# Kernel tuning notes

Hardware: AMD Instinct MI355X
Metric: run time of the kernel (lower is better)

## Reference

```python
import jax, jax.numpy as jnp
import numpy as np

N = 100000       # num nodes
E = 1600000      # num edges (avg degree 16)
IN_DIM = 256
EMB_DIM = 128
K = 2            # nlayers: number of propagation steps


def setup_inputs() -> dict:
    key = jax.random.key(0)
    k1, k2, k3, k4, k5 = jax.random.split(key, 5)
    x = jax.random.normal(k1, (N, IN_DIM), dtype=jnp.float32)
    # glorot-initialized linear weight + zero bias
    scale = jnp.sqrt(6.0 / (IN_DIM + EMB_DIM))
    W = jax.random.uniform(k2, (IN_DIM, EMB_DIM), minval=-scale, maxval=scale, dtype=jnp.float32)
    b = jnp.zeros((EMB_DIM,), dtype=jnp.float32)
    edge_src = jax.random.randint(k3, (E,), 0, N, dtype=jnp.int32)
    edge_dst = jax.random.randint(k4, (E,), 0, N, dtype=jnp.int32)
    # normalized-adjacency-like edge weights (positive, ~1/deg scale)
    edge_w = jax.random.uniform(k5, (E,), dtype=jnp.float32) * (1.0 / 16.0)
    return {"x": x, "W": W, "b": b, "edge_src": edge_src, "edge_dst": edge_dst, "edge_w": edge_w}


def reference(x, W, b, edge_src, edge_dst, edge_w):
    # dropout is identity in eval mode; linear + relu
    h = jax.nn.relu(x @ W + b)  # [N, EMB_DIM]
    # k-step sparse propagation: h <- g @ h, g given as COO edge list
    for _ in range(K):
        msg = h[edge_src] * edge_w[:, None]                     # [E, EMB_DIM]
        h = jax.ops.segment_sum(msg, edge_dst, num_segments=N)  # [N, EMB_DIM]
    return h
```

## Files before the change

### kernel.cpp

```cpp
#include <hip/hip_runtime.h>

#define IN_DIM 256
#define EMB 128
#define BKT_SHIFT 9
#define BKT_NODES 512
#define BINE 4096
#define SCAP 12288

typedef __attribute__((ext_vector_type(8))) short short8;
typedef __attribute__((ext_vector_type(4))) float f32x4;

__device__ __forceinline__ unsigned short bf16rtne(float f) {
    unsigned int u = __float_as_uint(f);
    return (unsigned short)((u + 0x7fffu + ((u >> 16) & 1u)) >> 16);
}

__device__ __forceinline__ unsigned int packbf2(float lo, float hi) {
    return ((unsigned int)bf16rtne(hi) << 16) | (unsigned int)bf16rtne(lo);
}

__device__ __forceinline__ short8 pack8(float4 f0, float4 f1) {
    union { uint4 u; short8 s; } U;
    asm("v_cvt_pk_bf16_f32 %0, %1, %2" : "=v"(U.u.x) : "v"(f0.x), "v"(f0.y));
    asm("v_cvt_pk_bf16_f32 %0, %1, %2" : "=v"(U.u.y) : "v"(f0.z), "v"(f0.w));
    asm("v_cvt_pk_bf16_f32 %0, %1, %2" : "=v"(U.u.z) : "v"(f1.x), "v"(f1.y));
    asm("v_cvt_pk_bf16_f32 %0, %1, %2" : "=v"(U.u.w) : "v"(f1.z), "v"(f1.w));
    return U.s;
}


__global__ __launch_bounds__(256) void bucket_hist(const int* __restrict__ dst,
                                                   int* __restrict__ ghist, int E) {
    __shared__ int h[256];
    int t = threadIdx.x;
    h[t] = 0;
    __syncthreads();
    int e0 = blockIdx.x * 1024;
    int e1 = min(E, e0 + 1024);
    for (int i = e0 + t; i < e1; i += 256) atomicAdd(&h[dst[i] >> BKT_SHIFT], 1);
    __syncthreads();
    if (h[t]) atomicAdd(&ghist[t], h[t]);
}

__global__ __launch_bounds__(256) void bucket_scan(const int* __restrict__ ghist,
                                                   int* __restrict__ bucket_off,
                                                   int* __restrict__ gcursor,
                                                   int* __restrict__ row_ptr,
                                                   int NB, int N, int E) {
    __shared__ int s[256];
    int t = threadIdx.x;
    int v = (t < NB) ? ghist[t] : 0;
    s[t] = v;
    __syncthreads();
    for (int off = 1; off < 256; off <<= 1) {
        int u = (t >= off) ? s[t - off] : 0;
        __syncthreads();
        s[t] += u;
        __syncthreads();
    }
    int excl = s[t] - v;
    if (t < NB) {
        bucket_off[t] = excl;
        gcursor[t] = excl;
    }
    if (t == 0) {
        bucket_off[NB] = E;
        row_ptr[N] = E;
    }
}


__global__ __launch_bounds__(512) void bin_scatter(const int* __restrict__ src,
                                                   const int* __restrict__ dst,
                                                   const float* __restrict__ w,
                                                   int* __restrict__ gcursor,
                                                   int2* __restrict__ binned, int E) {
    __shared__ int h[256];
    __shared__ int lbase[256];
    __shared__ int gbase[256];
    __shared__ int lcur[256];
    __shared__ int2 stage[BINE];
    __shared__ unsigned char sb[BINE];
    int t = threadIdx.x;
    int e0 = blockIdx.x * BINE;
    int e1 = min(E, e0 + BINE);
    int n = e1 - e0;

    int ed[8], es[8];
    float ewv[8];
#pragma unroll
    for (int j = 0; j < 8; ++j) {
        int i = e0 + t + j * 512;
        if (i < e1) {
            ed[j] = dst[i];
            es[j] = src[i];
            ewv[j] = w[i];
        } else
            ed[j] = -1;
    }
    if (t < 256) h[t] = 0;
    __syncthreads();
#pragma unroll
    for (int j = 0; j < 8; ++j)
        if (ed[j] >= 0) atomicAdd(&h[ed[j] >> BKT_SHIFT], 1);
    __syncthreads();
    int v = 0;
    if (t < 256) {
        v = h[t];
        lbase[t] = v;
    }
    __syncthreads();
    for (int off = 1; off < 256; off <<= 1) {
        int u = 0;
        if (t < 256 && t >= off) u = lbase[t - off];
        __syncthreads();
        if (t < 256) lbase[t] += u;
        __syncthreads();
    }
    if (t < 256) {
        lbase[t] -= v;
        lcur[t] = lbase[t];
        gbase[t] = v ? atomicAdd(&gcursor[t], v) : 0;
    }
    __syncthreads();
#pragma unroll
    for (int j = 0; j < 8; ++j) {
        if (ed[j] >= 0) {
            int b = ed[j] >> BKT_SHIFT;
            int p = atomicAdd(&lcur[b], 1);
            int2 r;
            r.x = es[j] | ((ed[j] & (BKT_NODES - 1)) << 17);
            r.y = __float_as_int(ewv[j]);
            stage[p] = r;
            sb[p] = (unsigned char)b;
        }
    }
    __syncthreads();
    for (int i = t; i < n; i += 512) {
        int b = sb[i];
        binned[gbase[b] + (i - lbase[b])] = stage[i];
    }
}


__global__ __launch_bounds__(1024) void bucket_sort(const int2* __restrict__ binned,
                                                    const int* __restrict__ bucket_off,
                                                    int2* __restrict__ sorted,
                                                    int* __restrict__ row_ptr, int N) {
    __shared__ int cnt[BKT_NODES];
    __shared__ int cur[BKT_NODES];
    __shared__ int scn[BKT_NODES];
    __shared__ int2 stage[SCAP];
    int t = threadIdx.x;
    int b = blockIdx.x;
    int node0 = b << BKT_SHIFT;
    int nn = min(BKT_NODES, N - node0);
    int beg = bucket_off[b];
    int endb = bucket_off[b + 1];
    int n = endb - beg;
    if (t < BKT_NODES) cnt[t] = 0;
    __syncthreads();
    for (int i = beg + t; i < endb; i += 1024) {
        int ld = ((unsigned int)binned[i].x) >> 17;
        atomicAdd(&cnt[ld], 1);
    }
    __syncthreads();
    int v = 0;
    if (t < BKT_NODES) {
        v = cnt[t];
        scn[t] = v;
    }
    __syncthreads();
    for (int off = 1; off < BKT_NODES; off <<= 1) {
        int u = 0;
        if (t < BKT_NODES && t >= off) u = scn[t - off];
        __syncthreads();
        if (t < BKT_NODES) scn[t] += u;
        __syncthreads();
    }
    if (t < BKT_NODES) {
        int excl = scn[t] - v;
        cur[t] = excl;
        if (t < nn) row_ptr[node0 + t] = beg + excl;
    }
    __syncthreads();
    if (n <= SCAP) {
        for (int i = beg + t; i < endb; i += 1024) {
            int2 r = binned[i];
            int ld = ((unsigned int)r.x) >> 17;
            int p = atomicAdd(&cur[ld], 1);
            r.x &= 0x1FFFF;
            stage[p] = r;
        }
        __syncthreads();
        for (int i = t; i < n; i += 1024) sorted[beg + i] = stage[i];
    } else {
        for (int i = beg + t; i < endb; i += 1024) {
            int2 r = binned[i];
            int ld = ((unsigned int)r.x) >> 17;
            int p = atomicAdd(&cur[ld], 1);
            r.x &= 0x1FFFF;
            sorted[beg + p] = r;
        }
    }
}


__global__ __launch_bounds__(256) void wt_cast(const float* __restrict__ W,
                                               unsigned short* __restrict__ wtg) {
    int i = blockIdx.x * 256 + threadIdx.x;
    int c = i & 127;
    int k = i >> 7;
    wtg[c * 256 + k] = bf16rtne(W[(size_t)k * 128 + c]);
}


__global__ __launch_bounds__(256) void x_cast(const float* __restrict__ x,
                                              unsigned short* __restrict__ xb, int total8) {
    int stride = gridDim.x * 256;
    for (int i = blockIdx.x * 256 + threadIdx.x; i < total8; i += stride) {
        const float4* s = (const float4*)(x + (size_t)i * 8);
        *(short8*)(xb + (size_t)i * 8) = pack8(s[0], s[1]);
    }
}


__global__ __launch_bounds__(256) void gemm_mfma(const unsigned short* __restrict__ xb,
                                                 const unsigned short* __restrict__ wtg,
                                                 const float* __restrict__ bias,
                                                 unsigned short* __restrict__ hbf, int N) {
    __shared__ unsigned short As[128][64];
    __shared__ unsigned short Bs[128][64];
    int tid = threadIdx.x;
    int wv = tid >> 6;
    int lane = tid & 63;
    int lr = lane & 15;
    int lg = lane >> 4;
    int wr = wv * 32;
    int row0 = blockIdx.x * 128;

    f32x4 acc[2][8];
#pragma unroll
    for (int m = 0; m < 2; ++m)
#pragma unroll
        for (int n = 0; n < 8; ++n) acc[m][n] = (f32x4){0.f, 0.f, 0.f, 0.f};

    int p0 = wv * 4 * 64 + lane;

    for (int kb = 0; kb < IN_DIM; kb += 64) {
#pragma unroll
        for (int i = 0; i < 4; ++i) {
            int p = p0 + i * 64;
            int r = p >> 3;
            int c = p & 7;
            int cs = (c ^ (r & 7)) * 8;
            int gr = row0 + r;
            if (gr >= N) gr = N - 1;
            const unsigned short* ga = xb + (size_t)gr * IN_DIM + kb + cs;
            __builtin_amdgcn_global_load_lds(
                (const __attribute__((address_space(1))) void*)ga,
                (__attribute__((address_space(3))) void*)((char*)&As[0][0] + (size_t)(wv * 4 + i) * 1024),
                16, 0, 0);
            const unsigned short* gb = wtg + (size_t)r * IN_DIM + kb + cs;
            __builtin_amdgcn_global_load_lds(
                (const __attribute__((address_space(1))) void*)gb,
                (__attribute__((address_space(3))) void*)((char*)&Bs[0][0] + (size_t)(wv * 4 + i) * 1024),
                16, 0, 0);
        }
        __syncthreads();

        short8 a[2][2];
#pragma unroll
        for (int m = 0; m < 2; ++m)
#pragma unroll
            for (int kk = 0; kk < 2; ++kk) {
                int r = wr + m * 16 + lr;
                int ch = kk * 4 + lg;
                a[m][kk] = *(const short8*)&As[r][((ch ^ (r & 7)) * 8)];
            }
#pragma unroll
        for (int n = 0; n < 8; ++n) {
            int cc = n * 16 + lr;
            int sw = cc & 7;
            short8 b0 = *(const short8*)&Bs[cc][(((0 * 4 + lg) ^ sw) * 8)];
            short8 b1 = *(const short8*)&Bs[cc][(((1 * 4 + lg) ^ sw) * 8)];
            acc[0][n] = __builtin_amdgcn_mfma_f32_16x16x32_bf16(a[0][0], b0, acc[0][n], 0, 0, 0);
            acc[0][n] = __builtin_amdgcn_mfma_f32_16x16x32_bf16(a[0][1], b1, acc[0][n], 0, 0, 0);
            acc[1][n] = __builtin_amdgcn_mfma_f32_16x16x32_bf16(a[1][0], b0, acc[1][n], 0, 0, 0);
            acc[1][n] = __builtin_amdgcn_mfma_f32_16x16x32_bf16(a[1][1], b1, acc[1][n], 0, 0, 0);
        }
        __syncthreads();
    }

#pragma unroll
    for (int n = 0; n < 8; ++n) {
        int c = n * 16 + lr;
        float bv = bias[c];
#pragma unroll
        for (int m = 0; m < 2; ++m) {
#pragma unroll
            for (int j = 0; j < 4; ++j) {
                int r = row0 + wr + m * 16 + lg * 4 + j;
                if (r < N) {
                    float v = fmaxf(acc[m][n][j] + bv, 0.f);
                    hbf[(size_t)r * EMB + c] = bf16rtne(v);
                }
            }
        }
    }
}


template <int OUTBF>
__global__ __launch_bounds__(256) void prop_g(const unsigned int* __restrict__ hin,
                                              void* __restrict__ hout,
                                              const int* __restrict__ rp,
                                              const int2* __restrict__ rec, int N) {
    int wvid = threadIdx.x >> 6;
    int lane = threadIdx.x & 63;
    int node = blockIdx.x * 4 + wvid;
    if (node >= N) return;
    int beg = __builtin_amdgcn_readfirstlane(rp[node]);
    int end = __builtin_amdgcn_readfirstlane(rp[node + 1]);
    float ax = 0.f, ay = 0.f;
    for (int c0 = beg; c0 < end; c0 += 64) {
        int cnt = end - c0;
        if (cnt > 64) cnt = 64;
        int li = lane < cnt ? lane : 0;
        int2 r = rec[c0 + li];
        for (int jb = 0; jb < cnt; jb += 8) {
            int ssrc[8];
            float sw[8];
#pragma unroll
            for (int k = 0; k < 8; ++k) {
                int jj = jb + k;
                int jc = jj < cnt ? jj : 0;
                ssrc[k] = __builtin_amdgcn_readlane(r.x, jc);
                float wv = __uint_as_float((unsigned int)__builtin_amdgcn_readlane(r.y, jc));
                sw[k] = (jj < cnt) ? wv : 0.f;
            }
            unsigned int g[8];
#pragma unroll
            for (int k = 0; k < 8; ++k) g[k] = hin[(size_t)ssrc[k] * 64 + lane];
#pragma unroll
            for (int k = 0; k < 8; ++k) {
                ax = fmaf(sw[k], __uint_as_float(g[k] << 16), ax);
                ay = fmaf(sw[k], __uint_as_float(g[k] & 0xffff0000u), ay);
            }
        }
    }
    if (OUTBF) {
        ((unsigned int*)hout)[(size_t)node * 64 + lane] = packbf2(ax, ay);
    } else {
        float2 o;
        o.x = ax;
        o.y = ay;
        ((float2*)hout)[(size_t)node * 64 + lane] = o;
    }
}


extern "C" void kernel_launch(void* const* d_in, const int* in_sizes, int n_in,
                              void* d_out, int out_size, void* d_ws, size_t ws_size,
                              hipStream_t stream) {
    const float* x = (const float*)d_in[0];
    const float* W = (const float*)d_in[1];
    const float* b = (const float*)d_in[2];
    const int* esrc = (const int*)d_in[3];
    const int* edst = (const int*)d_in[4];
    const float* ew = (const float*)d_in[5];
    int N = in_sizes[0] / IN_DIM;
    int E = in_sizes[3];
    int NB = (N + BKT_NODES - 1) >> BKT_SHIFT;

    char* p = (char*)d_ws;
    auto alloc = [&](size_t bytes) -> void* {
        void* r = (void*)p;
        p += (bytes + 255) & ~(size_t)255;
        return r;
    };
    unsigned short* hbf = (unsigned short*)alloc((size_t)N * EMB * 2);
    unsigned short* h1bf = (unsigned short*)alloc((size_t)N * EMB * 2);
    unsigned short* wtg = (unsigned short*)alloc((size_t)IN_DIM * EMB * 2);
    unsigned short* xbf = (unsigned short*)alloc((size_t)N * IN_DIM * 2);
    int* ghist = (int*)alloc(256 * 4);
    int* gcursor = (int*)alloc(256 * 4);
    int* bucket_off = (int*)alloc((size_t)(NB + 1) * 4);
    int* row_ptr = (int*)alloc((size_t)(N + 1) * 4);
    int2* binned = (int2*)alloc((size_t)E * 8);
    int2* sorted = (int2*)alloc((size_t)E * 8);

    hipMemsetAsync(ghist, 0, 256 * 4, stream);
    wt_cast<<<(IN_DIM * EMB) / 256, 256, 0, stream>>>(W, wtg);
    x_cast<<<2048, 256, 0, stream>>>(x, xbf, N * IN_DIM / 8);
    bucket_hist<<<(E + 1023) / 1024, 256, 0, stream>>>(edst, ghist, E);
    bucket_scan<<<1, 256, 0, stream>>>(ghist, bucket_off, gcursor, row_ptr, NB, N, E);
    bin_scatter<<<(E + BINE - 1) / BINE, 512, 0, stream>>>(esrc, edst, ew, gcursor, binned, E);
    bucket_sort<<<NB, 1024, 0, stream>>>(binned, bucket_off, sorted, row_ptr, N);

    gemm_mfma<<<(N + 127) / 128, 256, 0, stream>>>(xbf, wtg, b, hbf, N);
    prop_g<1><<<(N + 3) / 4, 256, 0, stream>>>((const unsigned int*)hbf, h1bf, row_ptr, sorted, N);
    prop_g<0><<<(N + 3) / 4, 256, 0, stream>>>((const unsigned int*)h1bf, d_out, row_ptr, sorted, N);
}
```

Measured before the change: 242.7 us.

## Fuse cast and histogram kernels into one prep kernel; restructure gather loop

The W transpose-cast, x bf16 cast and destination-bucket histogram kernels are merged into a single grid-stride prep kernel, removing two launches and their serialization gaps. The propagation kernel now handles edges in chunks of 16. Each lane loads the edge records directly, a uniform address, instead of one coalesced load followed by readlane broadcasts, and it issues 16 independent row gathers before accumulating. This gives more loads in flight per wave at the cost of more registers and redundant scalar-like record loads.

```diff
diff --git a/kernel.cpp b/kernel.cpp
--- a/kernel.cpp
+++ b/kernel.cpp
@@ -29,15 +29,28 @@
 }
 
 
-__global__ __launch_bounds__(256) void bucket_hist(const int* __restrict__ dst,
-                                                   int* __restrict__ ghist, int E) {
+__global__ __launch_bounds__(256) void prep(const float* __restrict__ W,
+                                            unsigned short* __restrict__ wtg,
+                                            const float* __restrict__ x,
+                                            unsigned short* __restrict__ xb, int total8,
+                                            const int* __restrict__ dst,
+                                            int* __restrict__ ghist, int E) {
+    int t = threadIdx.x;
+    int gsz = gridDim.x * 256;
+    int gid = blockIdx.x * 256 + t;
+    for (int i = gid; i < IN_DIM * EMB; i += gsz) {
+        int c = i & 127;
+        int k = i >> 7;
+        wtg[c * 256 + k] = bf16rtne(W[(size_t)k * 128 + c]);
+    }
+    for (int i = gid; i < total8; i += gsz) {
+        const float4* s = (const float4*)(x + (size_t)i * 8);
+        *(short8*)(xb + (size_t)i * 8) = pack8(s[0], s[1]);
+    }
     __shared__ int h[256];
-    int t = threadIdx.x;
     h[t] = 0;
     __syncthreads();
-    int e0 = blockIdx.x * 1024;
-    int e1 = min(E, e0 + 1024);
-    for (int i = e0 + t; i < e1; i += 256) atomicAdd(&h[dst[i] >> BKT_SHIFT], 1);
+    for (int i = gid; i < E; i += gsz) atomicAdd(&h[dst[i] >> BKT_SHIFT], 1);
     __syncthreads();
     if (h[t]) atomicAdd(&ghist[t], h[t]);
 }
@@ -202,25 +215,6 @@
             r.x &= 0x1FFFF;
             sorted[beg + p] = r;
         }
-    }
-}
-
-
-__global__ __launch_bounds__(256) void wt_cast(const float* __restrict__ W,
-                                               unsigned short* __restrict__ wtg) {
-    int i = blockIdx.x * 256 + threadIdx.x;
-    int c = i & 127;
-    int k = i >> 7;
-    wtg[c * 256 + k] = bf16rtne(W[(size_t)k * 128 + c]);
-}
-
-
-__global__ __launch_bounds__(256) void x_cast(const float* __restrict__ x,
-                                              unsigned short* __restrict__ xb, int total8) {
-    int stride = gridDim.x * 256;
-    for (int i = blockIdx.x * 256 + threadIdx.x; i < total8; i += stride) {
-        const float4* s = (const float4*)(x + (size_t)i * 8);
-        *(short8*)(xb + (size_t)i * 8) = pack8(s[0], s[1]);
     }
 }
 
@@ -323,30 +317,22 @@
     int beg = __builtin_amdgcn_readfirstlane(rp[node]);
     int end = __builtin_amdgcn_readfirstlane(rp[node + 1]);
     float ax = 0.f, ay = 0.f;
-    for (int c0 = beg; c0 < end; c0 += 64) {
+    for (int c0 = beg; c0 < end; c0 += 16) {
         int cnt = end - c0;
-        if (cnt > 64) cnt = 64;
-        int li = lane < cnt ? lane : 0;
-        int2 r = rec[c0 + li];
-        for (int jb = 0; jb < cnt; jb += 8) {
-            int ssrc[8];
-            float sw[8];
-#pragma unroll
-            for (int k = 0; k < 8; ++k) {
-                int jj = jb + k;
-                int jc = jj < cnt ? jj : 0;
-                ssrc[k] = __builtin_amdgcn_readlane(r.x, jc);
-                float wv = __uint_as_float((unsigned int)__builtin_amdgcn_readlane(r.y, jc));
-                sw[k] = (jj < cnt) ? wv : 0.f;
-            }
-            unsigned int g[8];
-#pragma unroll
-            for (int k = 0; k < 8; ++k) g[k] = hin[(size_t)ssrc[k] * 64 + lane];
-#pragma unroll
-            for (int k = 0; k < 8; ++k) {
-                ax = fmaf(sw[k], __uint_as_float(g[k] << 16), ax);
-                ay = fmaf(sw[k], __uint_as_float(g[k] & 0xffff0000u), ay);
-            }
+        if (cnt > 16) cnt = 16;
+        unsigned g[16];
+        float w[16];
+#pragma unroll
+        for (int k = 0; k < 16; ++k) {
+            int idx = c0 + (k < cnt ? k : cnt - 1);
+            int2 r = rec[idx];
+            w[k] = (k < cnt) ? __int_as_float(r.y) : 0.f;
+            g[k] = hin[(size_t)r.x * 64 + lane];
+        }
+#pragma unroll
+        for (int k = 0; k < 16; ++k) {
+            ax = fmaf(w[k], __uint_as_float(g[k] << 16), ax);
+            ay = fmaf(w[k], __uint_as_float(g[k] & 0xffff0000u), ay);
         }
     }
     if (OUTBF) {
@@ -391,9 +377,7 @@
     int2* sorted = (int2*)alloc((size_t)E * 8);
 
     hipMemsetAsync(ghist, 0, 256 * 4, stream);
-    wt_cast<<<(IN_DIM * EMB) / 256, 256, 0, stream>>>(W, wtg);
-    x_cast<<<2048, 256, 0, stream>>>(x, xbf, N * IN_DIM / 8);
-    bucket_hist<<<(E + 1023) / 1024, 256, 0, stream>>>(edst, ghist, E);
+    prep<<<2048, 256, 0, stream>>>(W, wtg, x, xbf, N * IN_DIM / 8, edst, ghist, E);
     bucket_scan<<<1, 256, 0, stream>>>(ghist, bucket_off, gcursor, row_ptr, NB, N, E);
     bin_scatter<<<(E + BINE - 1) / BINE, 512, 0, stream>>>(esrc, edst, ew, gcursor, binned, E);
     bucket_sort<<<NB, 1024, 0, stream>>>(binned, bucket_off, sorted, row_ptr, N);
```

New measurement: 265.3 us. 9.3% more time.
